# Optimization experiments

Hardware: AMD Instinct MI355X
Metric: run time of the kernel (lower is better)

## Reference

```python
import jax, jax.numpy as jnp
import numpy as np

NEG_INF = jnp.float32(-9e15)  # matches torch's -9e15 zero_vec
ALPHA = 0.2  # LeakyReLU negative slope


def setup_inputs() -> dict:
    key = jax.random.key(0)
    k1, k2, k3, k4, k5 = jax.random.split(key, 5)
    B, N, DIN, DOUT = 8, 2048, 128, 64
    h = jax.random.normal(k1, (B, N, DIN), dtype=jnp.float32)
    adj = jax.random.randint(k2, (B, N, N), 0, 2).astype(jnp.int32)
    mask = jax.random.randint(k3, (B, N), 0, 2).astype(jnp.int32)
    # learned params: W is nn.Linear(dim_in, dim_out, bias=False) -> store as [DIN, DOUT]
    W = jax.random.normal(k4, (DIN, DOUT), dtype=jnp.float32) / np.sqrt(DIN)
    # a is [2*dim_out, 1] in torch; store flat [2*DOUT]
    a = jax.random.normal(k5, (2 * DOUT,), dtype=jnp.float32) * 0.1
    return {"h": h, "adj": adj, "mask": mask, "W": W, "a": a}


def reference(h, adj, mask, W, a):
    # h: [B,N,DIN], adj: [B,N,N] int, mask: [B,N] int, W: [DIN,DOUT], a: [2*DOUT]
    dout = W.shape[1]
    z = h @ W  # [B,N,DOUT]
    # e_ij = LeakyReLU([z_i||z_j] . a) = LeakyReLU(z_i.a1 + z_j.a2)
    a1, a2 = a[:dout], a[dout:]
    s1 = jnp.einsum("bnd,d->bn", z, a1)  # contribution of source node i
    s2 = jnp.einsum("bnd,d->bn", z, a2)  # contribution of target node j
    e = jax.nn.leaky_relu(s1[:, :, None] + s2[:, None, :], negative_slope=ALPHA)  # [B,N,N]
    att = jnp.where(adj > 0, e, NEG_INF)
    mask2d = mask[:, :, None] * mask[:, None, :]  # [B,N,N]
    att = jnp.where(mask2d > 0, att, NEG_INF)
    att = jax.nn.softmax(att, axis=-1)
    h_prime = jnp.einsum("bij,bjd->bid", att, z)  # [B,N,DOUT]
    return jax.nn.elu(h_prime)  # concat=True path
```

## Files before the change

### kernel.cpp

```cpp
#include <hip/hip_runtime.h>

#define BB 8
#define NN 2048
#define DIN 128
#define DOUT 64
#define ALPHA_NS 0.2f
#define ITILE 16
#define JTILE 64
#define NWAVE 4
#define TTOT (NN / (JTILE * NWAVE))

typedef __attribute__((ext_vector_type(4))) int int4v;
typedef __attribute__((ext_vector_type(4))) short short4v;
typedef __attribute__((ext_vector_type(4))) unsigned short ushort4v;
typedef __attribute__((ext_vector_type(4))) float float4v;

__device__ __forceinline__ unsigned short f32_to_bf16_rne(float x) {
  unsigned u = __builtin_bit_cast(unsigned, x);
  u += 0x7FFFu + ((u >> 16) & 1u);
  return (unsigned short)(u >> 16);
}

__global__ __launch_bounds__(256, 4) void gat_zproj(
    const float* __restrict__ h, const float* __restrict__ W,
    const float* __restrict__ a, const int* __restrict__ mask,
    unsigned short* __restrict__ zF, float* __restrict__ s1,
    float* __restrict__ s2) {
  __shared__ float shbuf[6144];
  const int tid = threadIdx.x;
  const int w = tid >> 6, lane = tid & 63;
  const int zbid = blockIdx.x;
  const long r0 = (long)zbid * 16;
  float (*hS)[DIN] = reinterpret_cast<float(*)[DIN]>(shbuf);
  float (*accW)[16][DOUT] =
      reinterpret_cast<float(*)[16][DOUT]>(shbuf + 16 * DIN);

  float Wr[32];
#pragma unroll
  for (int kk = 0; kk < 32; ++kk) Wr[kk] = W[(w * 32 + kk) * DOUT + lane];

  {
    const int r = tid >> 4, c = (tid & 15) * 8;
    const float* src = h + (r0 + r) * DIN + c;
    *reinterpret_cast<float4*>(&hS[r][c]) = *reinterpret_cast<const float4*>(src);
    *reinterpret_cast<float4*>(&hS[r][c + 4]) =
        *reinterpret_cast<const float4*>(src + 4);
  }
  __syncthreads();

#pragma unroll
  for (int r = 0; r < 16; ++r) {
    float acc = 0.f;
#pragma unroll
    for (int k4 = 0; k4 < 8; ++k4) {
      const float4 h4 = *reinterpret_cast<const float4*>(&hS[r][w * 32 + k4 * 4]);
      acc = fmaf(h4.x, Wr[k4 * 4 + 0], acc);
      acc = fmaf(h4.y, Wr[k4 * 4 + 1], acc);
      acc = fmaf(h4.z, Wr[k4 * 4 + 2], acc);
      acc = fmaf(h4.w, Wr[k4 * 4 + 3], acc);
    }
    accW[w][r][lane] = acc;
  }
  __syncthreads();

  unsigned short zt4[4];
#pragma unroll
  for (int it = 0; it < 4; ++it) {
    const int i = w * 4 + it;
    const int d = lane;
    const float zv =
        accW[0][i][d] + accW[1][i][d] + accW[2][i][d] + accW[3][i][d];
    zt4[it] = f32_to_bf16_rne(zv);
    float v1 = zv * a[d];
    float v2 = zv * a[DOUT + d];
#pragma unroll
    for (int off = 32; off; off >>= 1) {
      v1 += __shfl_xor(v1, off);
      v2 += __shfl_xor(v2, off);
    }
    if (lane == 0) {
      s1[r0 + i] = v1;
      s2[r0 + i] = (mask[r0 + i] > 0) ? v2 : -30000.0f;
    }
  }
  {
    const int b = zbid >> 7;
    const int bloc = zbid & 127;
    const int jb = bloc >> 2;
    const int ks = bloc & 3;
    const int dt = lane >> 4, row16 = lane & 15;
    ushort4v v;
    v.x = zt4[0]; v.y = zt4[1]; v.z = zt4[2]; v.w = zt4[3];
    const size_t e = ((size_t)(b * 32 + jb)) * 4096 +
                     (size_t)(((dt * 4 + ks) * 64 + w * 16 + row16) * 4);
    *reinterpret_cast<ushort4v*>(zF + e) = v;
  }
}

__global__ __launch_bounds__(256, 4) void gat_attn(
    const unsigned short* __restrict__ zF, const float* __restrict__ s1g,
    const float* __restrict__ s2g, const int* __restrict__ adj,
    const int* __restrict__ mask, float* __restrict__ out) {
  const int lid = (blockIdx.x & 7) * 128 + (blockIdx.x >> 3);
  const int b = lid >> 7;
  const int i0 = (lid & 127) * ITILE;
  const int tid = threadIdx.x;
  const int w = tid >> 6, lane = tid & 63;
  const int row16 = lane & 15, kgrp = lane >> 4;
  const int rq = lane >> 4;
  const int jq = (lane & 15) * 4;

  __shared__ __align__(16) unsigned short pA[NWAVE][ITILE][72];
  __shared__ float accS[NWAVE][ITILE][DOUT];
  __shared__ float Lred[NWAVE][ITILE];

  float s1q[4];
  unsigned mbits = 0;
#pragma unroll
  for (int q = 0; q < 4; ++q) {
    s1q[q] = s1g[b * NN + i0 + q * 4 + rq];
    mbits |= (mask[b * NN + i0 + q * 4 + rq] > 0 ? 1u : 0u) << q;
  }

  float4v acc[5];
#pragma unroll
  for (int dt = 0; dt < 5; ++dt) acc[dt] = (float4v){0.f, 0.f, 0.f, 0.f};

  const short4v ones =
      (row16 == 0) ? short4v{(short)0x3F80, (short)0x3F80, (short)0x3F80,
                             (short)0x3F80}
                   : short4v{0, 0, 0, 0};

  const int* abase = adj + (size_t)(b * NN + i0) * NN;
  const unsigned short* ztb = zF + (size_t)(b * 32) * 4096 + lane * 4;

  int4v adjq[4];
#pragma unroll
  for (int q = 0; q < 4; ++q)
    adjq[q] = *reinterpret_cast<const int4v*>(
        abase + (size_t)(q * 4 + rq) * NN + w * JTILE + jq);
  float4 s2v = *reinterpret_cast<const float4*>(s2g + b * NN + w * JTILE + jq);
  short4v bfr[16];
  {
    const unsigned short* t0 = ztb + (size_t)w * 4096;
#pragma unroll
    for (int ks = 0; ks < 4; ++ks)
#pragma unroll
      for (int dt = 0; dt < 4; ++dt)
        bfr[ks * 4 + dt] = __builtin_bit_cast(
            short4v,
            *reinterpret_cast<const ushort4v*>(t0 + (dt * 4 + ks) * 256));
  }

#pragma unroll 1
  for (int t = 0; t < TTOT; ++t) {
#pragma unroll
    for (int q = 0; q < 4; ++q) {
      float sc0 = s1q[q] + s2v.x;
      float sc1 = s1q[q] + s2v.y;
      float sc2 = s1q[q] + s2v.z;
      float sc3 = s1q[q] + s2v.w;
      sc0 = fmaxf(sc0, ALPHA_NS * sc0);
      sc1 = fmaxf(sc1, ALPHA_NS * sc1);
      sc2 = fmaxf(sc2, ALPHA_NS * sc2);
      sc3 = fmaxf(sc3, ALPHA_NS * sc3);
      float p0 = (adjq[q].x > 0) ? __expf(sc0) : 0.f;
      float p1 = (adjq[q].y > 0) ? __expf(sc1) : 0.f;
      float p2 = (adjq[q].z > 0) ? __expf(sc2) : 0.f;
      float p3 = (adjq[q].w > 0) ? __expf(sc3) : 0.f;
      if (!((mbits >> q) & 1u)) {
        p0 = p1 = p2 = p3 = 1.0f;
      }
      unsigned lo, hi;
      asm("v_cvt_pk_bf16_f32 %0, %1, %2" : "=v"(lo) : "v"(p0), "v"(p1));
      asm("v_cvt_pk_bf16_f32 %0, %1, %2" : "=v"(hi) : "v"(p2), "v"(p3));
      uint2 pk; pk.x = lo; pk.y = hi;
      *reinterpret_cast<uint2*>(&pA[w][q * 4 + rq][jq]) = pk;
    }
    if (t + 1 < TTOT) {
      const int j0n = ((t + 1) * NWAVE + w) * JTILE;
#pragma unroll
      for (int q = 0; q < 4; ++q)
        adjq[q] = *reinterpret_cast<const int4v*>(
            abase + (size_t)(q * 4 + rq) * NN + j0n + jq);
      s2v = *reinterpret_cast<const float4*>(s2g + b * NN + j0n + jq);
    }
    const unsigned short* tn = ztb + (size_t)((t + 1) * NWAVE + w) * 4096;
    __builtin_amdgcn_s_setprio(1);
#pragma unroll
    for (int ks = 0; ks < 2; ++ks) {
      const short4v af = __builtin_bit_cast(
          short4v,
          *reinterpret_cast<const ushort4v*>(&pA[w][row16][ks * 16 + kgrp * 4]));
      acc[4] =
          __builtin_amdgcn_mfma_f32_16x16x16bf16_1k(af, ones, acc[4], 0, 0, 0);
#pragma unroll
      for (int dt = 0; dt < 4; ++dt)
        acc[dt] = __builtin_amdgcn_mfma_f32_16x16x16bf16_1k(af, bfr[ks * 4 + dt],
                                                            acc[dt], 0, 0, 0);
    }
    __builtin_amdgcn_s_setprio(0);
    if (t + 1 < TTOT) {
#pragma unroll
      for (int ks = 0; ks < 2; ++ks)
#pragma unroll
        for (int dt = 0; dt < 4; ++dt)
          bfr[ks * 4 + dt] = __builtin_bit_cast(
              short4v,
              *reinterpret_cast<const ushort4v*>(tn + (dt * 4 + ks) * 256));
    }
    __builtin_amdgcn_s_setprio(1);
#pragma unroll
    for (int ks = 2; ks < 4; ++ks) {
      const short4v af = __builtin_bit_cast(
          short4v,
          *reinterpret_cast<const ushort4v*>(&pA[w][row16][ks * 16 + kgrp * 4]));
      acc[4] =
          __builtin_amdgcn_mfma_f32_16x16x16bf16_1k(af, ones, acc[4], 0, 0, 0);
#pragma unroll
      for (int dt = 0; dt < 4; ++dt)
        acc[dt] = __builtin_amdgcn_mfma_f32_16x16x16bf16_1k(af, bfr[ks * 4 + dt],
                                                            acc[dt], 0, 0, 0);
    }
    __builtin_amdgcn_s_setprio(0);
    if (t + 1 < TTOT) {
#pragma unroll
      for (int ks = 2; ks < 4; ++ks)
#pragma unroll
        for (int dt = 0; dt < 4; ++dt)
          bfr[ks * 4 + dt] = __builtin_bit_cast(
              short4v,
              *reinterpret_cast<const ushort4v*>(tn + (dt * 4 + ks) * 256));
    }
  }

  if (row16 == 0) {
#pragma unroll
    for (int r = 0; r < 4; ++r) Lred[w][kgrp * 4 + r] = acc[4][r];
  }
#pragma unroll
  for (int dt = 0; dt < 4; ++dt) {
#pragma unroll
    for (int r = 0; r < 4; ++r)
      accS[w][kgrp * 4 + r][dt * 16 + row16] = acc[dt][r];
  }
  __syncthreads();

#pragma unroll
  for (int it = 0; it < 4; ++it) {
    const int i = (tid >> 6) + it * 4;
    const int d = tid & 63;
    const float L = Lred[0][i] + Lred[1][i] + Lred[2][i] + Lred[3][i];
    const float v = accS[0][i][d] + accS[1][i][d] + accS[2][i][d] + accS[3][i][d];
    const float hp = v / L;
    const float r = hp > 0.f ? hp : (__expf(hp) - 1.f);
    out[((long)b * NN + i0 + i) * DOUT + d] = r;
  }
}

extern "C" void kernel_launch(void* const* d_in, const int* in_sizes, int n_in,
                              void* d_out, int out_size, void* d_ws, size_t ws_size,
                              hipStream_t stream) {
  const float* h = (const float*)d_in[0];
  const int* adj = (const int*)d_in[1];
  const int* mask = (const int*)d_in[2];
  const float* W = (const float*)d_in[3];
  const float* a = (const float*)d_in[4];
  float* out = (float*)d_out;

  unsigned short* zF = (unsigned short*)d_ws;
  float* s1 = (float*)((char*)d_ws + (size_t)BB * NN * DOUT * 2);
  float* s2 = s1 + (size_t)BB * NN;

  gat_zproj<<<dim3(1024), dim3(256), 0, stream>>>(h, W, a, mask, zF, s1, s2);
  gat_attn<<<dim3(NN / ITILE * BB), dim3(256), 0, stream>>>(zF, s1, s2, adj,
                                                            mask, out);
}
```

Baseline: 43.19 us.

## Compute attention probabilities directly in MFMA A-fragment layout, drop LDS staging

Each lane now computes probabilities for its own MFMA A-operand row and k-slice, so the packed bf16 values feed the matrix instructions straight from registers instead of going through a shared-memory tile. The softmax denominator is summed in registers and reduced with cross-lane shuffles, replacing the extra MFMA against a ones vector. Adjacency loads become nontemporal. The aim is to remove LDS writes and reads and the per-row-sum MFMAs, at the cost of more s2 loads per lane and extra VALU adds.

```diff
diff --git a/kernel.cpp b/kernel.cpp
--- a/kernel.cpp
+++ b/kernel.cpp
@@ -107,39 +107,33 @@
   const int tid = threadIdx.x;
   const int w = tid >> 6, lane = tid & 63;
   const int row16 = lane & 15, kgrp = lane >> 4;
-  const int rq = lane >> 4;
-  const int jq = (lane & 15) * 4;
-
-  __shared__ __align__(16) unsigned short pA[NWAVE][ITILE][72];
+
   __shared__ float accS[NWAVE][ITILE][DOUT];
   __shared__ float Lred[NWAVE][ITILE];
 
-  float s1q[4];
-  unsigned mbits = 0;
-#pragma unroll
-  for (int q = 0; q < 4; ++q) {
-    s1q[q] = s1g[b * NN + i0 + q * 4 + rq];
-    mbits |= (mask[b * NN + i0 + q * 4 + rq] > 0 ? 1u : 0u) << q;
-  }
-
-  float4v acc[5];
-#pragma unroll
-  for (int dt = 0; dt < 5; ++dt) acc[dt] = (float4v){0.f, 0.f, 0.f, 0.f};
-
-  const short4v ones =
-      (row16 == 0) ? short4v{(short)0x3F80, (short)0x3F80, (short)0x3F80,
-                             (short)0x3F80}
-                   : short4v{0, 0, 0, 0};
-
-  const int* abase = adj + (size_t)(b * NN + i0) * NN;
+  const float s1v = s1g[b * NN + i0 + row16];
+  const bool iunm = (mask[b * NN + i0 + row16] > 0);
+
+  float4v acc[4];
+#pragma unroll
+  for (int dt = 0; dt < 4; ++dt) acc[dt] = (float4v){0.f, 0.f, 0.f, 0.f};
+  float lpart = 0.f;
+
+  const int* aln = adj + (size_t)(b * NN + i0 + row16) * NN + kgrp * 4;
+  const float* s2ln = s2g + b * NN + kgrp * 4;
   const unsigned short* ztb = zF + (size_t)(b * 32) * 4096 + lane * 4;
 
   int4v adjq[4];
-#pragma unroll
-  for (int q = 0; q < 4; ++q)
-    adjq[q] = *reinterpret_cast<const int4v*>(
-        abase + (size_t)(q * 4 + rq) * NN + w * JTILE + jq);
-  float4 s2v = *reinterpret_cast<const float4*>(s2g + b * NN + w * JTILE + jq);
+  float4 s2q[4];
+  {
+    const int j0 = w * JTILE;
+#pragma unroll
+    for (int ks = 0; ks < 4; ++ks) {
+      adjq[ks] = __builtin_nontemporal_load(
+          reinterpret_cast<const int4v*>(aln + j0 + ks * 16));
+      s2q[ks] = *reinterpret_cast<const float4*>(s2ln + j0 + ks * 16);
+    }
+  }
   short4v bfr[16];
   {
     const unsigned short* t0 = ztb + (size_t)w * 4096;
@@ -154,51 +148,53 @@
 
 #pragma unroll 1
   for (int t = 0; t < TTOT; ++t) {
-#pragma unroll
-    for (int q = 0; q < 4; ++q) {
-      float sc0 = s1q[q] + s2v.x;
-      float sc1 = s1q[q] + s2v.y;
-      float sc2 = s1q[q] + s2v.z;
-      float sc3 = s1q[q] + s2v.w;
+    short4v af[4];
+#pragma unroll
+    for (int ks = 0; ks < 4; ++ks) {
+      float sc0 = s1v + s2q[ks].x;
+      float sc1 = s1v + s2q[ks].y;
+      float sc2 = s1v + s2q[ks].z;
+      float sc3 = s1v + s2q[ks].w;
       sc0 = fmaxf(sc0, ALPHA_NS * sc0);
       sc1 = fmaxf(sc1, ALPHA_NS * sc1);
       sc2 = fmaxf(sc2, ALPHA_NS * sc2);
       sc3 = fmaxf(sc3, ALPHA_NS * sc3);
-      float p0 = (adjq[q].x > 0) ? __expf(sc0) : 0.f;
-      float p1 = (adjq[q].y > 0) ? __expf(sc1) : 0.f;
-      float p2 = (adjq[q].z > 0) ? __expf(sc2) : 0.f;
-      float p3 = (adjq[q].w > 0) ? __expf(sc3) : 0.f;
-      if (!((mbits >> q) & 1u)) {
+      float p0 = (adjq[ks].x > 0) ? __expf(sc0) : 0.f;
+      float p1 = (adjq[ks].y > 0) ? __expf(sc1) : 0.f;
+      float p2 = (adjq[ks].z > 0) ? __expf(sc2) : 0.f;
+      float p3 = (adjq[ks].w > 0) ? __expf(sc3) : 0.f;
+      if (!iunm) {
         p0 = p1 = p2 = p3 = 1.0f;
       }
       unsigned lo, hi;
       asm("v_cvt_pk_bf16_f32 %0, %1, %2" : "=v"(lo) : "v"(p0), "v"(p1));
       asm("v_cvt_pk_bf16_f32 %0, %1, %2" : "=v"(hi) : "v"(p2), "v"(p3));
-      uint2 pk; pk.x = lo; pk.y = hi;
-      *reinterpret_cast<uint2*>(&pA[w][q * 4 + rq][jq]) = pk;
+      lpart += __builtin_bit_cast(float, lo << 16) +
+               __builtin_bit_cast(float, lo & 0xFFFF0000u) +
+               __builtin_bit_cast(float, hi << 16) +
+               __builtin_bit_cast(float, hi & 0xFFFF0000u);
+      uint2 u;
+      u.x = lo;
+      u.y = hi;
+      af[ks] = __builtin_bit_cast(short4v, u);
     }
     if (t + 1 < TTOT) {
       const int j0n = ((t + 1) * NWAVE + w) * JTILE;
 #pragma unroll
-      for (int q = 0; q < 4; ++q)
-        adjq[q] = *reinterpret_cast<const int4v*>(
-            abase + (size_t)(q * 4 + rq) * NN + j0n + jq);
-      s2v = *reinterpret_cast<const float4*>(s2g + b * NN + j0n + jq);
+      for (int ks = 0; ks < 4; ++ks) {
+        adjq[ks] = __builtin_nontemporal_load(
+            reinterpret_cast<const int4v*>(aln + j0n + ks * 16));
+        s2q[ks] = *reinterpret_cast<const float4*>(s2ln + j0n + ks * 16);
+      }
     }
     const unsigned short* tn = ztb + (size_t)((t + 1) * NWAVE + w) * 4096;
     __builtin_amdgcn_s_setprio(1);
 #pragma unroll
-    for (int ks = 0; ks < 2; ++ks) {
-      const short4v af = __builtin_bit_cast(
-          short4v,
-          *reinterpret_cast<const ushort4v*>(&pA[w][row16][ks * 16 + kgrp * 4]));
-      acc[4] =
-          __builtin_amdgcn_mfma_f32_16x16x16bf16_1k(af, ones, acc[4], 0, 0, 0);
+    for (int ks = 0; ks < 2; ++ks)
 #pragma unroll
       for (int dt = 0; dt < 4; ++dt)
-        acc[dt] = __builtin_amdgcn_mfma_f32_16x16x16bf16_1k(af, bfr[ks * 4 + dt],
-                                                            acc[dt], 0, 0, 0);
-    }
+        acc[dt] = __builtin_amdgcn_mfma_f32_16x16x16bf16_1k(
+            af[ks], bfr[ks * 4 + dt], acc[dt], 0, 0, 0);
     __builtin_amdgcn_s_setprio(0);
     if (t + 1 < TTOT) {
 #pragma unroll
@@ -211,17 +207,11 @@
     }
     __builtin_amdgcn_s_setprio(1);
 #pragma unroll
-    for (int ks = 2; ks < 4; ++ks) {
-      const short4v af = __builtin_bit_cast(
-          short4v,
-          *reinterpret_cast<const ushort4v*>(&pA[w][row16][ks * 16 + kgrp * 4]));
-      acc[4] =
-          __builtin_amdgcn_mfma_f32_16x16x16bf16_1k(af, ones, acc[4], 0, 0, 0);
+    for (int ks = 2; ks < 4; ++ks)
 #pragma unroll
       for (int dt = 0; dt < 4; ++dt)
-        acc[dt] = __builtin_amdgcn_mfma_f32_16x16x16bf16_1k(af, bfr[ks * 4 + dt],
-                                                            acc[dt], 0, 0, 0);
-    }
+        acc[dt] = __builtin_amdgcn_mfma_f32_16x16x16bf16_1k(
+            af[ks], bfr[ks * 4 + dt], acc[dt], 0, 0, 0);
     __builtin_amdgcn_s_setprio(0);
     if (t + 1 < TTOT) {
 #pragma unroll
@@ -234,10 +224,9 @@
     }
   }
 
-  if (row16 == 0) {
-#pragma unroll
-    for (int r = 0; r < 4; ++r) Lred[w][kgrp * 4 + r] = acc[4][r];
-  }
+  lpart += __shfl_xor(lpart, 16);
+  lpart += __shfl_xor(lpart, 32);
+  if (kgrp == 0) Lred[w][row16] = lpart;
 #pragma unroll
   for (int dt = 0; dt < 4; ++dt) {
 #pragma unroll
```

Measured after the change: 63.04 us. 45.9% more time.

## Split attention j-range in two blocks and reduce partials in a finalize kernel

Applied to the files above, without the earlier changes.

The attention kernel now splits the neighbor (j) dimension into two halves, which doubles the grid to 2048 blocks and halves each block's loop. It also raises the launch_bounds occupancy hint to 8 and aliases the pA and accS shared buffers to cut LDS use. Partial numerators and softmax denominators go to workspace, and a new gat_fin kernel sums the halves and applies the normalization and ELU. This buys more parallelism and occupancy for the adjacency stream, at the cost of an extra launch and a round trip of about 8MB of partials through global memory.

```diff
diff --git a/kernel.cpp b/kernel.cpp
--- a/kernel.cpp
+++ b/kernel.cpp
@@ -8,7 +8,7 @@
 #define ITILE 16
 #define JTILE 64
 #define NWAVE 4
-#define TTOT (NN / (JTILE * NWAVE))
+#define TTOT_H (1024 / (JTILE * NWAVE))
 
 typedef __attribute__((ext_vector_type(4))) int int4v;
 typedef __attribute__((ext_vector_type(4))) short short4v;
@@ -97,22 +97,28 @@
   }
 }
 
-__global__ __launch_bounds__(256, 4) void gat_attn(
+__global__ __launch_bounds__(256, 8) void gat_attn(
     const unsigned short* __restrict__ zF, const float* __restrict__ s1g,
     const float* __restrict__ s2g, const int* __restrict__ adj,
-    const int* __restrict__ mask, float* __restrict__ out) {
-  const int lid = (blockIdx.x & 7) * 128 + (blockIdx.x >> 3);
-  const int b = lid >> 7;
-  const int i0 = (lid & 127) * ITILE;
+    const int* __restrict__ mask, float* __restrict__ pacc,
+    float* __restrict__ pL) {
+  const int lid = (blockIdx.x & 7) * 256 + (blockIdx.x >> 3);
+  const int b = lid >> 8;
+  const int rem = lid & 255;
+  const int i0 = (rem >> 1) * ITILE;
+  const int jh = rem & 1;
   const int tid = threadIdx.x;
   const int w = tid >> 6, lane = tid & 63;
   const int row16 = lane & 15, kgrp = lane >> 4;
   const int rq = lane >> 4;
   const int jq = (lane & 15) * 4;
 
-  __shared__ __align__(16) unsigned short pA[NWAVE][ITILE][72];
-  __shared__ float accS[NWAVE][ITILE][DOUT];
-  __shared__ float Lred[NWAVE][ITILE];
+  __shared__ __align__(16) char smem[16640];
+  unsigned short (*pA)[ITILE][72] =
+      reinterpret_cast<unsigned short(*)[ITILE][72]>(smem);
+  float (*accS)[ITILE][DOUT] =
+      reinterpret_cast<float(*)[ITILE][DOUT]>(smem);
+  float (*Lred)[ITILE] = reinterpret_cast<float(*)[ITILE]>(smem + 16384);
 
   float s1q[4];
   unsigned mbits = 0;
@@ -131,15 +137,17 @@
                              (short)0x3F80}
                    : short4v{0, 0, 0, 0};
 
-  const int* abase = adj + (size_t)(b * NN + i0) * NN;
-  const unsigned short* ztb = zF + (size_t)(b * 32) * 4096 + lane * 4;
+  const int* abase = adj + (size_t)(b * NN + i0) * NN + jh * 1024;
+  const float* s2b = s2g + b * NN + jh * 1024;
+  const unsigned short* ztb =
+      zF + (size_t)(b * 32 + jh * 16) * 4096 + lane * 4;
 
   int4v adjq[4];
 #pragma unroll
   for (int q = 0; q < 4; ++q)
     adjq[q] = *reinterpret_cast<const int4v*>(
         abase + (size_t)(q * 4 + rq) * NN + w * JTILE + jq);
-  float4 s2v = *reinterpret_cast<const float4*>(s2g + b * NN + w * JTILE + jq);
+  float4 s2v = *reinterpret_cast<const float4*>(s2b + w * JTILE + jq);
   short4v bfr[16];
   {
     const unsigned short* t0 = ztb + (size_t)w * 4096;
@@ -153,7 +161,7 @@
   }
 
 #pragma unroll 1
-  for (int t = 0; t < TTOT; ++t) {
+  for (int t = 0; t < TTOT_H; ++t) {
 #pragma unroll
     for (int q = 0; q < 4; ++q) {
       float sc0 = s1q[q] + s2v.x;
@@ -177,13 +185,13 @@
       uint2 pk; pk.x = lo; pk.y = hi;
       *reinterpret_cast<uint2*>(&pA[w][q * 4 + rq][jq]) = pk;
     }
-    if (t + 1 < TTOT) {
+    if (t + 1 < TTOT_H) {
       const int j0n = ((t + 1) * NWAVE + w) * JTILE;
 #pragma unroll
       for (int q = 0; q < 4; ++q)
         adjq[q] = *reinterpret_cast<const int4v*>(
             abase + (size_t)(q * 4 + rq) * NN + j0n + jq);
-      s2v = *reinterpret_cast<const float4*>(s2g + b * NN + j0n + jq);
+      s2v = *reinterpret_cast<const float4*>(s2b + j0n + jq);
     }
     const unsigned short* tn = ztb + (size_t)((t + 1) * NWAVE + w) * 4096;
     __builtin_amdgcn_s_setprio(1);
@@ -200,7 +208,7 @@
                                                             acc[dt], 0, 0, 0);
     }
     __builtin_amdgcn_s_setprio(0);
-    if (t + 1 < TTOT) {
+    if (t + 1 < TTOT_H) {
 #pragma unroll
       for (int ks = 0; ks < 2; ++ks)
 #pragma unroll
@@ -223,7 +231,7 @@
                                                             acc[dt], 0, 0, 0);
     }
     __builtin_amdgcn_s_setprio(0);
-    if (t + 1 < TTOT) {
+    if (t + 1 < TTOT_H) {
 #pragma unroll
       for (int ks = 2; ks < 4; ++ks)
 #pragma unroll
@@ -233,6 +241,8 @@
               *reinterpret_cast<const ushort4v*>(tn + (dt * 4 + ks) * 256));
     }
   }
+
+  __syncthreads();
 
   if (row16 == 0) {
 #pragma unroll
@@ -252,10 +262,32 @@
     const int d = tid & 63;
     const float L = Lred[0][i] + Lred[1][i] + Lred[2][i] + Lred[3][i];
     const float v = accS[0][i][d] + accS[1][i][d] + accS[2][i][d] + accS[3][i][d];
-    const float hp = v / L;
-    const float r = hp > 0.f ? hp : (__expf(hp) - 1.f);
-    out[((long)b * NN + i0 + i) * DOUT + d] = r;
-  }
+    const size_t grow = (size_t)b * NN + i0 + i;
+    pacc[(size_t)jh * (BB * NN * DOUT) + grow * DOUT + d] = v;
+    if (d == 0) pL[jh * (BB * NN) + grow] = L;
+  }
+}
+
+__global__ __launch_bounds__(256) void gat_fin(const float* __restrict__ pacc,
+                                              const float* __restrict__ pL,
+                                              float* __restrict__ out) {
+  const int base = (blockIdx.x * 256 + threadIdx.x) * 4;
+  const int r = base >> 6;
+  const float L = pL[r] + pL[BB * NN + r];
+  const float4 v0 = *reinterpret_cast<const float4*>(pacc + (size_t)base);
+  const float4 v1 =
+      *reinterpret_cast<const float4*>(pacc + (size_t)(BB * NN * DOUT) + base);
+  const float rcpL = 1.0f / L;
+  float4 o;
+  o.x = (v0.x + v1.x) * rcpL;
+  o.y = (v0.y + v1.y) * rcpL;
+  o.z = (v0.z + v1.z) * rcpL;
+  o.w = (v0.w + v1.w) * rcpL;
+  o.x = o.x > 0.f ? o.x : (__expf(o.x) - 1.f);
+  o.y = o.y > 0.f ? o.y : (__expf(o.y) - 1.f);
+  o.z = o.z > 0.f ? o.z : (__expf(o.z) - 1.f);
+  o.w = o.w > 0.f ? o.w : (__expf(o.w) - 1.f);
+  *reinterpret_cast<float4*>(out + (size_t)base) = o;
 }
 
 extern "C" void kernel_launch(void* const* d_in, const int* in_sizes, int n_in,
@@ -271,8 +303,11 @@
   unsigned short* zF = (unsigned short*)d_ws;
   float* s1 = (float*)((char*)d_ws + (size_t)BB * NN * DOUT * 2);
   float* s2 = s1 + (size_t)BB * NN;
+  float* pacc = s2 + (size_t)BB * NN;
+  float* pL = pacc + (size_t)2 * BB * NN * DOUT;
 
   gat_zproj<<<dim3(1024), dim3(256), 0, stream>>>(h, W, a, mask, zF, s1, s2);
-  gat_attn<<<dim3(NN / ITILE * BB), dim3(256), 0, stream>>>(zF, s1, s2, adj,
-                                                            mask, out);
-}
+  gat_attn<<<dim3(2048), dim3(256), 0, stream>>>(zF, s1, s2, adj, mask, pacc,
+                                                 pL);
+  gat_fin<<<dim3(BB * NN * DOUT / 1024), dim3(256), 0, stream>>>(pacc, pL, out);
+}
```

Measured after the change: 140.0 us. +224.1%, slower.
